# Kernel tuning notes

Measured on AMD Instinct MI355X. Metric: run time of the kernel, lower is better.

The kernel has to match this reference:

```python
import jax, jax.numpy as jnp
import numpy as np

N = 50000
E = 800000
IN_DIM = 128
HID = 64
HEADS = 4
OUT_DIM = 128


def setup_inputs() -> dict:
    key = jax.random.key(0)
    ks = jax.random.split(key, 12)
    s = lambda fan: 1.0 / np.sqrt(fan)
    return {
        'features': jax.random.normal(ks[0], (N, IN_DIM), jnp.float32),
        'edge_index': jax.random.randint(ks[1], (2, E), 0, N, jnp.int64),
        # layer 1: in_dim -> heads*hid, concat=True
        'W1': jax.random.normal(ks[2], (IN_DIM, HEADS * HID), jnp.float32) * s(IN_DIM),
        'att_src1': jax.random.normal(ks[3], (HEADS, HID), jnp.float32) * s(HID),
        'att_dst1': jax.random.normal(ks[4], (HEADS, HID), jnp.float32) * s(HID),
        'bias1': jnp.zeros((HEADS * HID,), jnp.float32),
        # layer 2: heads*hid -> out_dim, 1 head, concat=False
        'W2': jax.random.normal(ks[5], (HEADS * HID, OUT_DIM), jnp.float32) * s(HEADS * HID),
        'att_src2': jax.random.normal(ks[6], (1, OUT_DIM), jnp.float32) * s(OUT_DIM),
        'att_dst2': jax.random.normal(ks[7], (1, OUT_DIM), jnp.float32) * s(OUT_DIM),
        'bias2': jnp.zeros((OUT_DIM,), jnp.float32),
    }


def _gat_conv(x, src, dst, W, a_src, a_dst, bias, heads, out_ch):
    n = x.shape[0]
    h = (x @ W).reshape(n, heads, out_ch)              # [N, H, C]
    alpha_s = jnp.einsum('nhc,hc->nh', h, a_src)       # [N, H]
    alpha_d = jnp.einsum('nhc,hc->nh', h, a_dst)
    e = jax.nn.leaky_relu(alpha_s[src] + alpha_d[dst], 0.2)  # [E, H]
    # segment softmax over incoming edges of each dst node
    m = jax.ops.segment_max(e, dst, num_segments=n)
    m = jnp.where(jnp.isfinite(m), m, 0.0)
    ex = jnp.exp(e - m[dst])
    denom = jax.ops.segment_sum(ex, dst, num_segments=n)
    alpha = ex / denom[dst]                            # [E, H]
    out = jax.ops.segment_sum(alpha[:, :, None] * h[src], dst, num_segments=n)  # [N, H, C]
    return out.reshape(n, heads * out_ch) + bias


def reference(features, edge_index, W1, att_src1, att_dst1, bias1, W2, att_src2, att_dst2, bias2):
    n = features.shape[0]
    loops = jnp.arange(n, dtype=edge_index.dtype)
    src = jnp.concatenate([edge_index[0], loops])
    dst = jnp.concatenate([edge_index[1], loops])

    act = lambda v: jax.nn.leaky_relu(v, 0.2)
    x = _gat_conv(features, src, dst, W1, att_src1, att_dst1, bias1, HEADS, HID)
    x = act(x)  # dropout inactive (eval)
    x = _gat_conv(x, src, dst, W2, att_src2, att_dst2, bias2, 1, OUT_DIM)
    x = act(x)
    # in_dim == out_dim -> identity residual
    return x + features
```

## Files before the change

kernel.cpp:

```cpp
#include <hip/hip_runtime.h>
#include <math.h>

#define LRELU(x) ((x) > 0.0f ? (x) : 0.2f * (x))

typedef __attribute__((ext_vector_type(8))) short bf16x8;
typedef __attribute__((ext_vector_type(4))) float floatx4;

__device__ __forceinline__ float bf2f(ushort u) {
    union { unsigned u; float f; } v; v.u = ((unsigned)u) << 16; return v.f;
}
__device__ __forceinline__ ushort f2bf(float f) {
    union { float f; unsigned u; } v; v.f = f;
    unsigned r = (v.u + 0x7FFFu + ((v.u >> 16) & 1u)) >> 16;
    return (ushort)r;
}

__global__ __launch_bounds__(256) void prep_kernel(
    const float* __restrict__ feat, const float* __restrict__ W1,
    const float* __restrict__ as1, const float* __restrict__ ad1,
    const float* __restrict__ W2, const float* __restrict__ as2,
    const float* __restrict__ ad2, const int* __restrict__ ei,
    ushort* __restrict__ featb, ushort* __restrict__ Bp1, ushort* __restrict__ Bp2,
    int* __restrict__ deg, ushort* __restrict__ col,
    int N, int E, int Npart, int b_fil, int b_cvt, int b_p1)
{
    const int b = blockIdx.x, t = threadIdx.x;
    if (b < b_fil) {
        const int fb = b;
        const int part = fb & 7;
        const int base = (fb >> 3) * 2048;
        const int lo = part * Npart;
        const int hi = min(N, lo + Npart);
        for (int q0 = 0; q0 < 8; q0 += 4) {
            int dsts[4]; bool val[4];
#pragma unroll
            for (int u = 0; u < 4; ++u) {
                int k = base + (q0 + u) * 256 + t;
                val[u] = k < E;
                if (val[u]) dsts[u] = ei[E + k];
            }
#pragma unroll
            for (int u = 0; u < 4; ++u) {
                if (val[u] && dsts[u] >= lo && dsts[u] < hi) {
                    int k = base + (q0 + u) * 256 + t;
                    int src = ei[k];
                    int slot = atomicAdd(&deg[dsts[u]], 1);
                    if (slot < 63) col[dsts[u] * 64 + slot] = (ushort)src;
                }
            }
        }
    } else if (b < b_fil + b_cvt) {
        int i = (b - b_fil) * 256 + t;
        if (i < N * 32) {
            float4 v = ((const float4*)feat)[i];
            ushort4 o;
            o.x = f2bf(v.x); o.y = f2bf(v.y); o.z = f2bf(v.z); o.w = f2bf(v.w);
            ((ushort4*)featb)[i] = o;
        }
    } else if (b < b_fil + b_cvt + b_p1) {
        int i = (b - b_fil - b_cvt) * 256 + t;
        if (i < 272 * 128) {
            int n = i / 128, k = i % 128;
            float v;
            if (n < 256) v = W1[k * 256 + n];
            else if (n < 260) {
                int h = n - 256; float s = 0.f;
                for (int c = 0; c < 64; ++c) s += W1[k * 256 + h * 64 + c] * as1[h * 64 + c];
                v = s;
            } else if (n < 264) {
                int h = n - 260; float s = 0.f;
                for (int c = 0; c < 64; ++c) s += W1[k * 256 + h * 64 + c] * ad1[h * 64 + c];
                v = s;
            } else v = 0.f;
            Bp1[i] = f2bf(v);
        }
    } else {
        int i = (b - b_fil - b_cvt - b_p1) * 256 + t;
        if (i < 144 * 256) {
            int n = i / 256, k = i % 256;
            float v;
            if (n < 128) v = W2[k * 128 + n];
            else if (n == 128) {
                float s = 0.f;
                for (int c = 0; c < 128; ++c) s += W2[k * 128 + c] * as2[c];
                v = s;
            } else if (n == 129) {
                float s = 0.f;
                for (int c = 0; c < 128; ++c) s += W2[k * 128 + c] * ad2[c];
                v = s;
            } else v = 0.f;
            Bp2[i] = f2bf(v);
        }
    }
}

__global__ __launch_bounds__(256) void gemm_attn1_kernel(
    const ushort* __restrict__ A, const ushort* __restrict__ Bp,
    float* __restrict__ as_, float* __restrict__ ad_, int M)
{
    const int lane = threadIdx.x & 63;
    const int wave = threadIdx.x >> 6;
    const int quad = lane >> 4;
    const int l16  = lane & 15;
    const int row0 = blockIdx.x * 64 + wave * 16;
    const int arow = min(row0 + l16, M - 1);
    const ushort* ap = A + (size_t)arow * 128 + quad * 8;
    const ushort* bp = Bp + (size_t)(256 + l16) * 128 + quad * 8;

    floatx4 acc = (floatx4){0.f, 0.f, 0.f, 0.f};
#pragma unroll
    for (int k0 = 0; k0 < 128; k0 += 32) {
        bf16x8 a = *(const bf16x8*)(ap + k0);
        bf16x8 b = *(const bf16x8*)(bp + k0);
        acc = __builtin_amdgcn_mfma_f32_16x16x32_bf16(a, b, acc, 0, 0, 0);
    }
#pragma unroll
    for (int r = 0; r < 4; ++r) {
        int row = row0 + quad * 4 + r;
        if (row < M) {
            float v = acc[r];
            if (l16 < 4)      as_[row * 4 + l16] = v;
            else if (l16 < 8) ad_[row * 4 + (l16 - 4)] = v;
        }
    }
}

__global__ __launch_bounds__(256) void gat_gather1_kernel(
    const int* __restrict__ deg, const ushort* __restrict__ col,
    const float* __restrict__ as_, const float* __restrict__ ad_,
    const ushort* __restrict__ xb, ushort* __restrict__ aggx, int N)
{
    __shared__ float4 alph[4][64];
    const int lane = threadIdx.x & 63;
    const int wave = threadIdx.x >> 6;
    const int n = blockIdx.x * 4 + wave;
    if (n >= N) return;
    const int dgE = min(deg[n], 63);
    const float4 ad4 = *(const float4*)(ad_ + n * 4);

    int src = n;
    float4 ex4 = {0.f, 0.f, 0.f, 0.f};
    if (lane <= dgE) {
        if (lane < dgE) src = col[n * 64 + lane];
        float4 a4 = *(const float4*)(as_ + src * 4);
        ex4.x = __expf(LRELU(a4.x + ad4.x));
        ex4.y = __expf(LRELU(a4.y + ad4.y));
        ex4.z = __expf(LRELU(a4.z + ad4.z));
        ex4.w = __expf(LRELU(a4.w + ad4.w));
        alph[wave][lane] = ex4;
    }
    float sx = ex4.x, sy = ex4.y, sz = ex4.z, sw = ex4.w;
#pragma unroll
    for (int m = 1; m < 64; m <<= 1) {
        sx += __shfl_xor(sx, m, 64); sy += __shfl_xor(sy, m, 64);
        sz += __shfl_xor(sz, m, 64); sw += __shfl_xor(sw, m, 64);
    }
    const float rd[4] = {1.0f / sx, 1.0f / sy, 1.0f / sz, 1.0f / sw};

    const int esl = lane >> 5;
    const int ch0 = (lane & 31) * 4;
    const int dg = dgE + 1;
    float acc[4][4] = {};
    for (int j0 = 0; j0 < dg; j0 += 8) {
        ushort4 u[4]; float4 a[4]; bool v[4]; int jj[4];
#pragma unroll
        for (int q = 0; q < 4; ++q) {
            jj[q] = j0 + 2 * q + esl;
            v[q] = jj[q] < dg;
            if (v[q]) {
                int s = __shfl(src, jj[q], 64);
                a[q] = alph[wave][jj[q]];
                u[q] = *(const ushort4*)(xb + (size_t)s * 128 + ch0);
            }
        }
#pragma unroll
        for (int q = 0; q < 4; ++q) {
            if (v[q]) {
                float f0 = bf2f(u[q].x), f1 = bf2f(u[q].y), f2 = bf2f(u[q].z), f3 = bf2f(u[q].w);
                acc[0][0] += a[q].x * f0; acc[0][1] += a[q].x * f1; acc[0][2] += a[q].x * f2; acc[0][3] += a[q].x * f3;
                acc[1][0] += a[q].y * f0; acc[1][1] += a[q].y * f1; acc[1][2] += a[q].y * f2; acc[1][3] += a[q].y * f3;
                acc[2][0] += a[q].z * f0; acc[2][1] += a[q].z * f1; acc[2][2] += a[q].z * f2; acc[2][3] += a[q].z * f3;
                acc[3][0] += a[q].w * f0; acc[3][1] += a[q].w * f1; acc[3][2] += a[q].w * f2; acc[3][3] += a[q].w * f3;
            }
        }
    }
#pragma unroll
    for (int h = 0; h < 4; ++h)
#pragma unroll
        for (int c = 0; c < 4; ++c) acc[h][c] += __shfl_xor(acc[h][c], 32, 64);

    if (lane < 32) {
#pragma unroll
        for (int h = 0; h < 4; ++h) {
            ushort4 o;
            o.x = f2bf(acc[h][0] * rd[h]); o.y = f2bf(acc[h][1] * rd[h]);
            o.z = f2bf(acc[h][2] * rd[h]); o.w = f2bf(acc[h][3] * rd[h]);
            *(ushort4*)(aggx + ((size_t)h * N + n) * 128 + ch0) = o;
        }
    }
}

__device__ __forceinline__ void l2_tile(int ct, const ushort x1s[64][264],
    const ushort* __restrict__ Bp2, int brow, int M, int lane,
    ushort* __restrict__ h2b, float* __restrict__ as2_, float* __restrict__ ad2_)
{
    const int quad = lane >> 4;
    const int l16  = lane & 15;
    bf16x8 bfr[8];
#pragma unroll
    for (int kq = 0; kq < 8; ++kq)
        bfr[kq] = *(const bf16x8*)(Bp2 + (size_t)(ct * 16 + l16) * 256 + kq * 32 + quad * 8);

    floatx4 acc[4];
#pragma unroll
    for (int rg = 0; rg < 4; ++rg) acc[rg] = (floatx4){0.f, 0.f, 0.f, 0.f};
#pragma unroll
    for (int kq = 0; kq < 8; ++kq) {
#pragma unroll
        for (int rg = 0; rg < 4; ++rg) {
            bf16x8 a = *(const bf16x8*)&x1s[rg * 16 + l16][kq * 32 + quad * 8];
            acc[rg] = __builtin_amdgcn_mfma_f32_16x16x32_bf16(a, bfr[kq], acc[rg], 0, 0, 0);
        }
    }
    if (ct < 8) {
#pragma unroll
        for (int rg = 0; rg < 4; ++rg)
#pragma unroll
            for (int r = 0; r < 4; ++r) {
                int row = brow + rg * 16 + quad * 4 + r;
                if (row < M) h2b[(size_t)row * 128 + ct * 16 + l16] = f2bf(acc[rg][r]);
            }
    } else {
#pragma unroll
        for (int rg = 0; rg < 4; ++rg)
#pragma unroll
            for (int r = 0; r < 4; ++r) {
                int row = brow + rg * 16 + quad * 4 + r;
                if (row < M) {
                    if (l16 == 0)      as2_[row] = acc[rg][r];
                    else if (l16 == 1) ad2_[row] = acc[rg][r];
                }
            }
    }
}

__global__ __launch_bounds__(256) void gemm_l1l2_kernel(
    const ushort* __restrict__ aggx, const ushort* __restrict__ Bp1,
    const float* __restrict__ bias1, const ushort* __restrict__ Bp2,
    ushort* __restrict__ h2b, float* __restrict__ as2_, float* __restrict__ ad2_, int M)
{
    __shared__ ushort x1s[64][264];
    const int lane = threadIdx.x & 63;
    const int wave = threadIdx.x >> 6;
    const int quad = lane >> 4;
    const int l16  = lane & 15;
    const int brow = blockIdx.x * 64;

    bf16x8 bfr[4][4];
#pragma unroll
    for (int nt = 0; nt < 4; ++nt)
#pragma unroll
        for (int kq = 0; kq < 4; ++kq)
            bfr[nt][kq] = *(const bf16x8*)(Bp1 + (size_t)(wave * 64 + nt * 16 + l16) * 128 + kq * 32 + quad * 8);

    bf16x8 afr[4][4];
#pragma unroll
    for (int rt = 0; rt < 4; ++rt) {
        const int arow = min(brow + rt * 16 + l16, M - 1);
        const ushort* ap = aggx + ((size_t)wave * M + arow) * 128 + quad * 8;
#pragma unroll
        for (int kq = 0; kq < 4; ++kq)
            afr[rt][kq] = *(const bf16x8*)(ap + kq * 32);
    }

#pragma unroll
    for (int rt = 0; rt < 4; ++rt) {
        floatx4 acc[4];
#pragma unroll
        for (int nt = 0; nt < 4; ++nt) acc[nt] = (floatx4){0.f, 0.f, 0.f, 0.f};
#pragma unroll
        for (int kq = 0; kq < 4; ++kq)
#pragma unroll
            for (int nt = 0; nt < 4; ++nt)
                acc[nt] = __builtin_amdgcn_mfma_f32_16x16x32_bf16(afr[rt][kq], bfr[nt][kq], acc[nt], 0, 0, 0);
#pragma unroll
        for (int nt = 0; nt < 4; ++nt) {
            const int c = wave * 64 + nt * 16 + l16;
            const float bv = bias1[c];
#pragma unroll
            for (int r = 0; r < 4; ++r)
                x1s[rt * 16 + quad * 4 + r][c] = f2bf(LRELU(acc[nt][r] + bv));
        }
    }
    __syncthreads();

    l2_tile(wave * 2,     x1s, Bp2, brow, M, lane, h2b, as2_, ad2_);
    l2_tile(wave * 2 + 1, x1s, Bp2, brow, M, lane, h2b, as2_, ad2_);
    if (wave == 3)
        l2_tile(8,        x1s, Bp2, brow, M, lane, h2b, as2_, ad2_);
}

__global__ __launch_bounds__(256) void gat_gather2_kernel(
    const int* __restrict__ deg, const ushort* __restrict__ col,
    const float* __restrict__ as_, const float* __restrict__ ad_,
    const ushort* __restrict__ h2, const float* __restrict__ bias,
    const float* __restrict__ resid, float* __restrict__ out, int N)
{
    __shared__ float alph[4][64];
    const int lane = threadIdx.x & 63;
    const int wave = threadIdx.x >> 6;
    const int n = blockIdx.x * 4 + wave;
    if (n >= N) return;
    const int dgE = min(deg[n], 63);
    const float adv = ad_[n];

    int src = n;
    float ex = 0.f;
    if (lane <= dgE) {
        if (lane < dgE) src = col[n * 64 + lane];
        ex = __expf(LRELU(as_[src] + adv));
        alph[wave][lane] = ex;
    }
    float s = ex;
#pragma unroll
    for (int m = 1; m < 64; m <<= 1) s += __shfl_xor(s, m, 64);
    const float rden = 1.0f / s;

    const int esl = lane >> 5;
    const int ch0 = (lane & 31) * 4;
    const int dg = dgE + 1;
    float ax = 0.f, ay = 0.f, az = 0.f, aw = 0.f;
    for (int j0 = 0; j0 < dg; j0 += 8) {
        ushort4 u[4]; float a[4]; bool v[4]; int jj[4];
#pragma unroll
        for (int q = 0; q < 4; ++q) {
            jj[q] = j0 + 2 * q + esl;
            v[q] = jj[q] < dg;
            if (v[q]) {
                int sA = __shfl(src, jj[q], 64);
                a[q] = alph[wave][jj[q]];
                u[q] = *(const ushort4*)(h2 + (size_t)sA * 128 + ch0);
            }
        }
#pragma unroll
        for (int q = 0; q < 4; ++q) {
            if (v[q]) {
                ax += a[q] * bf2f(u[q].x); ay += a[q] * bf2f(u[q].y);
                az += a[q] * bf2f(u[q].z); aw += a[q] * bf2f(u[q].w);
            }
        }
    }
    ax += __shfl_xor(ax, 32, 64); ay += __shfl_xor(ay, 32, 64);
    az += __shfl_xor(az, 32, 64); aw += __shfl_xor(aw, 32, 64);

    if (lane < 32) {
        const float4 bv = *(const float4*)(bias + ch0);
        const float4 fv = *(const float4*)(resid + (size_t)n * 128 + ch0);
        float4 o;
        o.x = LRELU(ax * rden + bv.x) + fv.x;
        o.y = LRELU(ay * rden + bv.y) + fv.y;
        o.z = LRELU(az * rden + bv.z) + fv.z;
        o.w = LRELU(aw * rden + bv.w) + fv.w;
        *(float4*)(out + (size_t)n * 128 + ch0) = o;
    }
}

extern "C" void kernel_launch(void* const* d_in, const int* in_sizes, int n_in,
                              void* d_out, int out_size, void* d_ws, size_t ws_size,
                              hipStream_t stream)
{
    const float* feat = (const float*)d_in[0];
    const int*   ei   = (const int*)d_in[1];
    const float* W1   = (const float*)d_in[2];
    const float* asrc1 = (const float*)d_in[3];
    const float* adst1 = (const float*)d_in[4];
    const float* bias1 = (const float*)d_in[5];
    const float* W2    = (const float*)d_in[6];
    const float* asrc2 = (const float*)d_in[7];
    const float* adst2 = (const float*)d_in[8];
    const float* bias2 = (const float*)d_in[9];
    float* outp = (float*)d_out;

    const int IN_DIM = 128, C2 = 128;
    const int N = in_sizes[0] / IN_DIM;
    const int E = in_sizes[1] / 2;

    char* w = (char*)d_ws;
    ushort* featb = (ushort*)w; w += (size_t)N * IN_DIM * 2;
    ushort* aggx  = (ushort*)w; w += (size_t)4 * N * IN_DIM * 2;
    ushort* h2b   = (ushort*)w; w += (size_t)N * C2 * 2;
    ushort* Bp1   = (ushort*)w; w += (size_t)272 * 128 * 2;
    ushort* Bp2   = (ushort*)w; w += (size_t)144 * 256 * 2;
    float* as1_   = (float*)w;  w += (size_t)N * 4 * 4;
    float* ad1_   = (float*)w;  w += (size_t)N * 4 * 4;
    float* as2_   = (float*)w;  w += (size_t)N * 4;
    float* ad2_   = (float*)w;  w += (size_t)N * 4;
    int* deg      = (int*)w;    w += (size_t)N * 4;
    ushort* col   = (ushort*)w; w += (size_t)N * 64 * 2;

    dim3 blk(256);
    const int mg = (N + 63) / 64;
    const int gg = (N + 3) / 4;
    const int Npart = (N + 7) / 8;

    const int b_cvt = (N * 32 + 255) / 256;
    const int b_p1  = (272 * 128 + 255) / 256;
    const int b_p2  = (144 * 256 + 255) / 256;
    const int b_fil = 8 * ((E + 2047) / 2048);

    hipMemsetAsync(deg, 0, (size_t)N * 4, stream);
    prep_kernel<<<dim3(b_fil + b_cvt + b_p1 + b_p2), blk, 0, stream>>>(
        feat, W1, asrc1, adst1, W2, asrc2, adst2, ei,
        featb, Bp1, Bp2, deg, col, N, E, Npart, b_fil, b_cvt, b_p1);

    gemm_attn1_kernel<<<dim3(mg), blk, 0, stream>>>(featb, Bp1, as1_, ad1_, N);
    gat_gather1_kernel<<<dim3(gg), blk, 0, stream>>>(deg, col, as1_, ad1_, featb, aggx, N);

    gemm_l1l2_kernel<<<dim3(mg), blk, 0, stream>>>(aggx, Bp1, bias1, Bp2, h2b, as2_, ad2_, N);

    gat_gather2_kernel<<<dim3(gg), blk, 0, stream>>>(deg, col, as2_, ad2_, h2b, bias2, feat, outp, N);
}
```

Before: 257.2 us.

## Remap gather kernels so each lane owns two channels of every edge

Both gather kernels switch from splitting edges across half-waves (each lane loading 4 channels) to having all 64 lanes read one full 128-channel row per edge, 2 channels per lane. Source indices go to LDS and are read back as wave-uniform scalars, and accumulation uses packed float2 math. This removes the final cross-half shuffle reduction, the per-edge shuffles and the idle half-wave on output. In exchange each load is narrower, 4 bytes per lane instead of 8, and the wave issues more load instructions per edge.

```diff
diff --git a/kernel.cpp b/kernel.cpp
--- a/kernel.cpp
+++ b/kernel.cpp
@@ -5,6 +5,7 @@
 
 typedef __attribute__((ext_vector_type(8))) short bf16x8;
 typedef __attribute__((ext_vector_type(4))) float floatx4;
+typedef __attribute__((ext_vector_type(2))) float f32x2;
 
 __device__ __forceinline__ float bf2f(ushort u) {
     union { unsigned u; float f; } v; v.u = ((unsigned)u) << 16; return v.f;
@@ -13,6 +14,11 @@
     union { float f; unsigned u; } v; v.f = f;
     unsigned r = (v.u + 0x7FFFu + ((v.u >> 16) & 1u)) >> 16;
     return (ushort)r;
+}
+__device__ __forceinline__ f32x2 bfpair(unsigned w) {
+    union { unsigned u; float f; } lo, hi;
+    lo.u = w << 16; hi.u = w & 0xffff0000u;
+    return (f32x2){lo.f, hi.f};
 }
 
 __global__ __launch_bounds__(256) void prep_kernel(
@@ -131,6 +137,7 @@
     const ushort* __restrict__ xb, ushort* __restrict__ aggx, int N)
 {
     __shared__ float4 alph[4][64];
+    __shared__ int    srcs[4][64];
     const int lane = threadIdx.x & 63;
     const int wave = threadIdx.x >> 6;
     const int n = blockIdx.x * 4 + wave;
@@ -142,6 +149,7 @@
     float4 ex4 = {0.f, 0.f, 0.f, 0.f};
     if (lane <= dgE) {
         if (lane < dgE) src = col[n * 64 + lane];
+        srcs[wave][lane] = src;
         float4 a4 = *(const float4*)(as_ + src * 4);
         ex4.x = __expf(LRELU(a4.x + ad4.x));
         ex4.y = __expf(LRELU(a4.y + ad4.y));
@@ -155,49 +163,46 @@
         sx += __shfl_xor(sx, m, 64); sy += __shfl_xor(sy, m, 64);
         sz += __shfl_xor(sz, m, 64); sw += __shfl_xor(sw, m, 64);
     }
-    const float rd[4] = {1.0f / sx, 1.0f / sy, 1.0f / sz, 1.0f / sw};
-
-    const int esl = lane >> 5;
-    const int ch0 = (lane & 31) * 4;
+    const float rd0 = 1.0f / sx, rd1 = 1.0f / sy, rd2 = 1.0f / sz, rd3 = 1.0f / sw;
+
     const int dg = dgE + 1;
-    float acc[4][4] = {};
+    const unsigned coff = lane * 2;
+    f32x2 acc0 = {0.f, 0.f}, acc1 = {0.f, 0.f}, acc2 = {0.f, 0.f}, acc3 = {0.f, 0.f};
+
     for (int j0 = 0; j0 < dg; j0 += 8) {
-        ushort4 u[4]; float4 a[4]; bool v[4]; int jj[4];
-#pragma unroll
-        for (int q = 0; q < 4; ++q) {
-            jj[q] = j0 + 2 * q + esl;
-            v[q] = jj[q] < dg;
-            if (v[q]) {
-                int s = __shfl(src, jj[q], 64);
-                a[q] = alph[wave][jj[q]];
-                u[q] = *(const ushort4*)(xb + (size_t)s * 128 + ch0);
-            }
-        }
-#pragma unroll
-        for (int q = 0; q < 4; ++q) {
-            if (v[q]) {
-                float f0 = bf2f(u[q].x), f1 = bf2f(u[q].y), f2 = bf2f(u[q].z), f3 = bf2f(u[q].w);
-                acc[0][0] += a[q].x * f0; acc[0][1] += a[q].x * f1; acc[0][2] += a[q].x * f2; acc[0][3] += a[q].x * f3;
-                acc[1][0] += a[q].y * f0; acc[1][1] += a[q].y * f1; acc[1][2] += a[q].y * f2; acc[1][3] += a[q].y * f3;
-                acc[2][0] += a[q].z * f0; acc[2][1] += a[q].z * f1; acc[2][2] += a[q].z * f2; acc[2][3] += a[q].z * f3;
-                acc[3][0] += a[q].w * f0; acc[3][1] += a[q].w * f1; acc[3][2] += a[q].w * f2; acc[3][3] += a[q].w * f3;
-            }
-        }
-    }
-#pragma unroll
-    for (int h = 0; h < 4; ++h)
-#pragma unroll
-        for (int c = 0; c < 4; ++c) acc[h][c] += __shfl_xor(acc[h][c], 32, 64);
-
-    if (lane < 32) {
-#pragma unroll
-        for (int h = 0; h < 4; ++h) {
-            ushort4 o;
-            o.x = f2bf(acc[h][0] * rd[h]); o.y = f2bf(acc[h][1] * rd[h]);
-            o.z = f2bf(acc[h][2] * rd[h]); o.w = f2bf(acc[h][3] * rd[h]);
-            *(ushort4*)(aggx + ((size_t)h * N + n) * 128 + ch0) = o;
-        }
-    }
+        unsigned u[8];
+#pragma unroll
+        for (int s = 0; s < 8; ++s) {
+            int jj = j0 + s;
+            if (jj < dg) {
+                int sa = __builtin_amdgcn_readfirstlane(srcs[wave][jj]);
+                u[s] = *(const unsigned*)(xb + (size_t)sa * 128 + coff);
+            }
+        }
+#pragma unroll
+        for (int s = 0; s < 8; ++s) {
+            int jj = j0 + s;
+            if (jj < dg) {
+                float4 a = alph[wave][jj];
+                f32x2 xv = bfpair(u[s]);
+                acc0 += (f32x2){a.x, a.x} * xv;
+                acc1 += (f32x2){a.y, a.y} * xv;
+                acc2 += (f32x2){a.z, a.z} * xv;
+                acc3 += (f32x2){a.w, a.w} * xv;
+            }
+        }
+    }
+
+    const size_t nb = (size_t)n * 128 + coff;
+    ushort2 o0, o1, o2, o3;
+    o0.x = f2bf(acc0.x * rd0); o0.y = f2bf(acc0.y * rd0);
+    o1.x = f2bf(acc1.x * rd1); o1.y = f2bf(acc1.y * rd1);
+    o2.x = f2bf(acc2.x * rd2); o2.y = f2bf(acc2.y * rd2);
+    o3.x = f2bf(acc3.x * rd3); o3.y = f2bf(acc3.y * rd3);
+    *(ushort2*)(aggx + nb)                      = o0;
+    *(ushort2*)(aggx + (size_t)N * 128 + nb)    = o1;
+    *(ushort2*)(aggx + (size_t)2 * N * 128 + nb) = o2;
+    *(ushort2*)(aggx + (size_t)3 * N * 128 + nb) = o3;
 }
 
 __device__ __forceinline__ void l2_tile(int ct, const ushort x1s[64][264],
@@ -307,6 +312,7 @@
     const float* __restrict__ resid, float* __restrict__ out, int N)
 {
     __shared__ float alph[4][64];
+    __shared__ int   srcs[4][64];
     const int lane = threadIdx.x & 63;
     const int wave = threadIdx.x >> 6;
     const int n = blockIdx.x * 4 + wave;
@@ -318,6 +324,7 @@
     float ex = 0.f;
     if (lane <= dgE) {
         if (lane < dgE) src = col[n * 64 + lane];
+        srcs[wave][lane] = src;
         ex = __expf(LRELU(as_[src] + adv));
         alph[wave][lane] = ex;
     }
@@ -326,43 +333,36 @@
     for (int m = 1; m < 64; m <<= 1) s += __shfl_xor(s, m, 64);
     const float rden = 1.0f / s;
 
-    const int esl = lane >> 5;
-    const int ch0 = (lane & 31) * 4;
     const int dg = dgE + 1;
-    float ax = 0.f, ay = 0.f, az = 0.f, aw = 0.f;
+    const unsigned coff = lane * 2;
+    f32x2 acc = {0.f, 0.f};
+
     for (int j0 = 0; j0 < dg; j0 += 8) {
-        ushort4 u[4]; float a[4]; bool v[4]; int jj[4];
-#pragma unroll
-        for (int q = 0; q < 4; ++q) {
-            jj[q] = j0 + 2 * q + esl;
-            v[q] = jj[q] < dg;
-            if (v[q]) {
-                int sA = __shfl(src, jj[q], 64);
-                a[q] = alph[wave][jj[q]];
-                u[q] = *(const ushort4*)(h2 + (size_t)sA * 128 + ch0);
-            }
-        }
-#pragma unroll
-        for (int q = 0; q < 4; ++q) {
-            if (v[q]) {
-                ax += a[q] * bf2f(u[q].x); ay += a[q] * bf2f(u[q].y);
-                az += a[q] * bf2f(u[q].z); aw += a[q] * bf2f(u[q].w);
-            }
-        }
-    }
-    ax += __shfl_xor(ax, 32, 64); ay += __shfl_xor(ay, 32, 64);
-    az += __shfl_xor(az, 32, 64); aw += __shfl_xor(aw, 32, 64);
-
-    if (lane < 32) {
-        const float4 bv = *(const float4*)(bias + ch0);
-        const float4 fv = *(const float4*)(resid + (size_t)n * 128 + ch0);
-        float4 o;
-        o.x = LRELU(ax * rden + bv.x) + fv.x;
-        o.y = LRELU(ay * rden + bv.y) + fv.y;
-        o.z = LRELU(az * rden + bv.z) + fv.z;
-        o.w = LRELU(aw * rden + bv.w) + fv.w;
-        *(float4*)(out + (size_t)n * 128 + ch0) = o;
-    }
+        unsigned u[8];
+#pragma unroll
+        for (int sI = 0; sI < 8; ++sI) {
+            int jj = j0 + sI;
+            if (jj < dg) {
+                int sa = __builtin_amdgcn_readfirstlane(srcs[wave][jj]);
+                u[sI] = *(const unsigned*)(h2 + (size_t)sa * 128 + coff);
+            }
+        }
+#pragma unroll
+        for (int sI = 0; sI < 8; ++sI) {
+            int jj = j0 + sI;
+            if (jj < dg) {
+                float a = alph[wave][jj];
+                acc += (f32x2){a, a} * bfpair(u[sI]);
+            }
+        }
+    }
+
+    const float2 bv = *(const float2*)(bias + coff);
+    const float2 fv = *(const float2*)(resid + (size_t)n * 128 + coff);
+    float2 o;
+    o.x = LRELU(acc.x * rden + bv.x) + fv.x;
+    o.y = LRELU(acc.y * rden + bv.y) + fv.y;
+    *(float2*)(out + (size_t)n * 128 + coff) = o;
 }
 
 extern "C" void kernel_launch(void* const* d_in, const int* in_sizes, int n_in,
```

Measured after the change: 298.4 us. +16.0%, slower.
